# Kernel optimization log

Measured on AMD Instinct MI355X. Metric: run time of the kernel, lower is better.

Reference implementation:

```python
import jax, jax.numpy as jnp
import numpy as np

NL = 64      # layers
NOBS = 400   # observed (velocity, period) pairs
NC = 3000    # trial phase velocities in Clist
DAMP = 1.0


def _var(p, q, ra, rb, wvno, xka, xkb, dpth):
    # surf96 'var': layer eigenfunction products, with c<v / c==v / c>v branches
    ra_s = jnp.where(ra > 0, ra, 1.0)
    rb_s = jnp.where(rb > 0, rb, 1.0)
    # P-wave branch
    sinp = jnp.sin(p)
    facp = jnp.where(p < 16.0, jnp.exp(-2.0 * p), 0.0)
    sinp_e = (1.0 - facp) * 0.5
    ltp = wvno < xka
    eqp = wvno == xka
    pex = jnp.where(ltp | eqp, 0.0, p)
    cosp = jnp.where(ltp, jnp.cos(p), jnp.where(eqp, 1.0, (1.0 + facp) * 0.5))
    w = jnp.where(ltp, sinp / ra_s, jnp.where(eqp, dpth, sinp_e / ra_s))
    x = jnp.where(ltp, -ra * sinp, jnp.where(eqp, 0.0, ra * sinp_e))
    # S-wave branch
    sinq = jnp.sin(q)
    facq = jnp.where(q < 16.0, jnp.exp(-2.0 * q), 0.0)
    sinq_e = (1.0 - facq) * 0.5
    lts = wvno < xkb
    eqs = wvno == xkb
    sex = jnp.where(lts | eqs, 0.0, q)
    cosq = jnp.where(lts, jnp.cos(q), jnp.where(eqs, 1.0, (1.0 + facq) * 0.5))
    y = jnp.where(lts, sinq / rb_s, jnp.where(eqs, dpth, sinq_e / rb_s))
    z = jnp.where(lts, -rb * sinq, jnp.where(eqs, 0.0, rb * sinq_e))

    exa = pex + sex
    a0 = jnp.where(exa < 60.0, jnp.exp(-exa), 0.0)
    return a0, cosp * cosq, cosp * y, cosp * z, cosq * w, cosq * x, x * y, x * z, w * y, w * z


def _dltar4(cvel, tper, d, a, b, rho):
    """Rayleigh dispersion determinant (Dunkin) for a flat batch of (c, T) pairs."""
    omega = jnp.maximum(2.0 * jnp.pi / tper, 1.0e-4)
    wvno = omega / cvel
    wvno2 = wvno * wvno

    def rs(v):
        xk = omega / v
        return xk, jnp.sqrt((wvno + xk) * jnp.abs(wvno - xk))

    # bottom half-space compound E vector
    xka, ra = rs(a[-1])
    xkb, rb = rs(b[-1])
    gammk = 2.0 * (b[-1] / omega) ** 2
    gam = gammk * wvno2
    gamm1 = gam - 1.0
    r = rho[-1]
    e = jnp.stack([
        r * r * (gamm1 * gamm1 - gam * gammk * ra * rb),
        -r * ra,
        r * (gamm1 - gammk * ra * rb),
        r * rb,
        wvno2 - ra * rb,
    ], axis=-1)  # [N,5]

    def step(e, lay):
        dm, am, bm, rm = lay
        xka, ra = rs(am)
        xkb, rb = rs(bm)
        gammk = 2.0 * (bm / omega) ** 2
        gam = gammk * wvno2
        p = ra * dm
        q = rb * dm
        a0, cpcq, cpy, cpz, cqw, cqx, xy, xz, wy, wz = _var(p, q, ra, rb, wvno, xka, xkb, dm)
        gamm1 = gam - 1.0
        twgm1 = gam + gamm1
        gmgmk = gam * gammk
        gmgm1 = gam * gamm1
        gm1sq = gamm1 * gamm1
        rho2 = rm * rm
        a0pq = a0 - cpcq
        t2 = -2.0 * wvno2
        # Dunkin 5x5 compound matrix (surf96 dnka)
        c00 = cpcq - 2.0 * gmgm1 * a0pq - gmgmk * xz - wvno2 * gm1sq * wy
        c01 = (wvno2 * cpy - cqx) / rm
        c02 = -(twgm1 * a0pq + gammk * xz + wvno2 * gamm1 * wy) / rm
        c03 = (cpz - wvno2 * cqw) / rm
        c04 = -(2.0 * wvno2 * a0pq + xz + wvno2 * wvno2 * wy) / rho2
        c10 = (gmgmk * cpz - gm1sq * cqw) * rm
        c11 = cpcq
        c12 = gammk * cpz - gamm1 * cqw
        c13 = -wz
        c14 = c03
        c30 = (gm1sq * cpy - gmgmk * cqx) * rm
        c31 = -xy
        c32 = gamm1 * cpy - gammk * cqx
        c33 = cpcq
        c34 = c01
        c40 = -(2.0 * gmgmk * gm1sq * a0pq + gmgmk * gmgmk * xz + gm1sq * gm1sq * wy) * rho2
        c41 = c30
        c42 = -(gmgm1 * twgm1 * a0pq + gam * gammk * gammk * xz + gamm1 * gm1sq * wy) * rm
        c43 = c10
        c44 = c00
        c20 = t2 * c42
        c21 = t2 * c32
        c22 = a0 + 2.0 * (cpcq - c00)
        c23 = t2 * c12
        c24 = t2 * c02
        ca = jnp.stack([
            jnp.stack([c00, c01, c02, c03, c04], axis=-1),
            jnp.stack([c10, c11, c12, c13, c14], axis=-1),
            jnp.stack([c20, c21, c22, c23, c24], axis=-1),
            jnp.stack([c30, c31, c32, c33, c34], axis=-1),
            jnp.stack([c40, c41, c42, c43, c44], axis=-1),
        ], axis=-2)  # [N,5,5]
        ee = jnp.einsum('nj,nji->ni', e, ca)
        nrm = jnp.max(jnp.abs(ee), axis=-1, keepdims=True)
        nrm = jnp.where(nrm < 1e-30, 1.0, nrm)  # surf96 normc
        return ee / nrm, None

    layers = (d[:-1], a[:-1], b[:-1], rho[:-1])
    e, _ = jax.lax.scan(step, e, layers, reverse=True)  # m = nL-2 ... 0 (llw = -1)
    return e[:, 0]


def _brocher(b):
    a = 0.9409 + 2.0947 * b - 0.8206 * b ** 2 + 0.2683 * b ** 3 - 0.0251 * b ** 4
    rho = 1.6612 * a - 0.4721 * a ** 2 + 0.0671 * a ** 3 - 0.0043 * a ** 4 + 0.000106 * a ** 5
    return a, rho


def _laplacian(n, dtype):
    L = 2.0 * jnp.eye(n, dtype=dtype) - jnp.eye(n, k=1, dtype=dtype) - jnp.eye(n, k=-1, dtype=dtype)
    return L.at[0, 0].set(1.0).at[n - 1, n - 1].set(1.0)


def _forward(vlist, tlist, d, b, Clist):
    a, rho = _brocher(b)  # initial_method='Brocher'
    e00 = _dltar4(vlist, tlist, d, a, b, rho)  # [N]
    # normalization grid: no_grad in original -> stop_gradient on all inputs
    sg = jax.lax.stop_gradient
    nC, nT = Clist.shape[0], tlist.shape[0]
    cgrid = jnp.repeat(Clist, nT)
    tgrid = jnp.tile(tlist, nC)
    det = _dltar4(sg(cgrid), sg(tgrid), sg(d), sg(a), sg(b), sg(rho)).reshape(nC, nT)
    rng = det.max(axis=0) - det.min(axis=0)  # [nT]
    e00 = e00 / rng
    # compress='exp' (torch: 0.1 ** abs(e00) - 1; normalized det branch is unused downstream)
    e00 = jnp.power(jnp.asarray(0.1, e00.dtype), jnp.abs(e00)) - 1.0
    e00_all = jnp.sum(jnp.abs(e00)) / e00.shape[0]
    L = _laplacian(b.shape[0], b.dtype)
    m_norm = DAMP * (L @ b) / b.shape[0]
    return e00_all + jnp.sum(jnp.abs(m_norm))


def setup_inputs() -> dict:
    key = jax.random.key(0)
    k1, k2 = jax.random.split(key)
    tlist = 0.5 + 19.5 * jax.random.uniform(k1, (NOBS,), dtype=jnp.float32)  # periods (s)
    vlist = 1.0 + 3.0 * jax.random.uniform(k2, (NOBS,), dtype=jnp.float32)   # phase velocities (km/s)
    d = jnp.full((NL,), 0.5, dtype=jnp.float32)                              # thicknesses (km)
    b = jnp.linspace(1.0, 4.5, NL, dtype=jnp.float32)                        # Vs profile (km/s)
    Clist = jnp.linspace(1.0, 4.0, NC, dtype=jnp.float32)                    # trial velocities
    return {"vlist": vlist, "tlist": tlist, "d": d, "b": b, "Clist": Clist}


def reference(vlist, tlist, d, b, Clist):
    return _forward(vlist, tlist, d, b, Clist)
```

## Files before the change

### kernel.cpp

```cpp
#include <hip/hip_runtime.h>
#include <math.h>
#include <float.h>

#define NL      64
#define NOBS    400
#define NC      3000
#define HALF_NC 1500
#define CHUNK   64
#define NCHUNK  24
#define TWO_PI_F   6.2831853071795864769f
#define INV_2PI_F  0.15915494309189535f
#define LOG2E_F    1.4426950408889634f
#define LOG2_0P1  -3.3219280948873623f

typedef float fx2 __attribute__((ext_vector_type(2)));

__device__ __forceinline__ float hsin(float x)  { return __builtin_amdgcn_sinf(x); }
__device__ __forceinline__ float hcos(float x)  { return __builtin_amdgcn_cosf(x); }
__device__ __forceinline__ float hexp2(float x) { return __builtin_amdgcn_exp2f(x); }
__device__ __forceinline__ float hrcp(float x)  { return __builtin_amdgcn_rcpf(x); }
__device__ __forceinline__ float hsqrt(float x) { return __builtin_amdgcn_sqrtf(x); }

__device__ __forceinline__ fx2 v_sqrt(fx2 v) { fx2 r; r.x = hsqrt(v.x); r.y = hsqrt(v.y); return r; }
__device__ __forceinline__ fx2 v_rcp (fx2 v) { fx2 r; r.x = hrcp(v.x);  r.y = hrcp(v.y);  return r; }
__device__ __forceinline__ fx2 v_sin (fx2 v) { fx2 r; r.x = hsin(v.x);  r.y = hsin(v.y);  return r; }
__device__ __forceinline__ fx2 v_cos (fx2 v) { fx2 r; r.x = hcos(v.x);  r.y = hcos(v.y);  return r; }
__device__ __forceinline__ fx2 v_exp2(fx2 v) { fx2 r; r.x = hexp2(v.x); r.y = hexp2(v.y); return r; }
__device__ __forceinline__ fx2 v_abs (fx2 v) { fx2 r; r.x = fabsf(v.x); r.y = fabsf(v.y); return r; }
__device__ __forceinline__ fx2 v_max (fx2 a, fx2 b) { fx2 r; r.x = fmaxf(a.x, b.x); r.y = fmaxf(a.y, b.y); return r; }

__device__ __forceinline__ unsigned enc(float f) {
    unsigned u = __float_as_uint(f);
    return (u & 0x80000000u) ? ~u : (u | 0x80000000u);
}
__device__ __forceinline__ float dec(unsigned k) {
    unsigned u = (k & 0x80000000u) ? (k & 0x7fffffffu) : ~k;
    return __uint_as_float(u);
}

__global__ void prep_kernel(const float* __restrict__ b, float* __restrict__ a_out,
                            float* __restrict__ rho_out,
                            unsigned* __restrict__ maxenc, unsigned* __restrict__ minenc) {
    int i = threadIdx.x;
    if (i < NL) {
        float bb = b[i];
        float b2 = bb * bb, b3 = b2 * bb, b4 = b3 * bb;
        float a = 0.9409f + 2.0947f * bb - 0.8206f * b2 + 0.2683f * b3 - 0.0251f * b4;
        float a2 = a * a, a3 = a2 * a, a4 = a3 * a, a5 = a4 * a;
        float rho = 1.6612f * a - 0.4721f * a2 + 0.0671f * a3 - 0.0043f * a4 + 0.000106f * a5;
        a_out[i] = a;
        rho_out[i] = rho;
    }
    for (int j = i; j < NOBS; j += 256) {
        maxenc[j] = 0u;
        minenc[j] = 0xFFFFFFFFu;
    }
}


struct SideVals { float cosv, wv, xv, fv; };

__device__ __forceinline__ SideVals side_mixed(float ra, bool lt, float dmsin,
                                               float dmexp, float ir) {
    float s = hsin(ra * dmsin);
    float c = hcos(ra * dmsin);
    float f = hexp2(ra * dmexp);
    float se = 0.5f - 0.5f * f;
    SideVals r;
    r.cosv = lt ? c : (0.5f + 0.5f * f);
    r.wv = (lt ? s : se) * ir;
    r.xv = ra * (lt ? -s : se);
    r.fv = lt ? 1.0f : f;
    return r;
}

template <bool NORM>
__device__ __forceinline__ void layer_step(
    fx2& f0, fx2& f1, fx2& f2, fx2& f3, fx2& f4,
    const float* __restrict__ P, fx2 wvno2, fx2 t2) {

    float xka2 = P[0], xkb2 = P[1], gammk = P[2];
    float dmsin = P[3], dmexp = P[4];
    float rr = P[5], rr2 = P[6];

    f1 *= rr; f2 *= rr; f3 *= rr; f4 *= rr2;

    fx2 ra2 = wvno2 - xka2;
    fx2 rb2 = wvno2 - xkb2;
    fx2 ra = v_sqrt(v_abs(ra2));
    fx2 rb = v_sqrt(v_abs(rb2));
    fx2 gam = gammk * wvno2;

    bool px = ra2.x < 0.0f, py = ra2.y < 0.0f;
    bool sx = rb2.x < 0.0f, sy = rb2.y < 0.0f;

    fx2 ra_s = v_max(ra, (fx2)1e-18f);
    fx2 rb_s = v_max(rb, (fx2)1e-18f);
    fx2 rp  = v_rcp(ra_s * rb_s);
    fx2 ira = rb_s * rp;
    fx2 irb = ra_s * rp;

    bool allP_prop = __all(px && py);
    bool allP_evan = __all(!(px || py));
    bool allS_prop = __all(sx && sy);
    bool allS_evan = __all(!(sx || sy));

    fx2 cosp, w, x, fp;
    if (allP_prop) {
        fx2 arg = ra * dmsin;
        fx2 s = v_sin(arg);
        cosp = v_cos(arg);
        w = s * ira;
        x = -(ra * s);
        fp = (fx2)1.0f;
    } else if (allP_evan) {
        fx2 f = v_exp2(ra * dmexp);
        fx2 se = 0.5f - 0.5f * f;
        cosp = 0.5f + 0.5f * f;
        w = se * ira;
        x = ra * se;
        fp = f;
    } else {
        SideVals vx = side_mixed(ra.x, px, dmsin, dmexp, ira.x);
        SideVals vy = side_mixed(ra.y, py, dmsin, dmexp, ira.y);
        cosp.x = vx.cosv; w.x = vx.wv; x.x = vx.xv; fp.x = vx.fv;
        cosp.y = vy.cosv; w.y = vy.wv; x.y = vy.xv; fp.y = vy.fv;
    }

    fx2 cosq, y, z, fq;
    if (allS_prop) {
        fx2 arg = rb * dmsin;
        fx2 s = v_sin(arg);
        cosq = v_cos(arg);
        y = s * irb;
        z = -(rb * s);
        fq = (fx2)1.0f;
    } else if (allS_evan) {
        fx2 f = v_exp2(rb * dmexp);
        fx2 se = 0.5f - 0.5f * f;
        cosq = 0.5f + 0.5f * f;
        y = se * irb;
        z = rb * se;
        fq = f;
    } else {
        SideVals vx = side_mixed(rb.x, sx, dmsin, dmexp, irb.x);
        SideVals vy = side_mixed(rb.y, sy, dmsin, dmexp, irb.y);
        cosq.x = vx.cosv; y.x = vx.wv; z.x = vx.xv; fq.x = vx.fv;
        cosq.y = vy.cosv; y.y = vy.wv; z.y = vy.xv; fq.y = vy.fv;
    }

    fx2 a0;
    if (allP_prop && allS_prop) {
        a0 = (fx2)1.0f;
    } else {
        a0 = v_sqrt(fp * fq);
    }

    fx2 cpcq = cosp * cosq;
    fx2 cpy = cosp * y, cpz = cosp * z;
    fx2 cqw = cosq * w, cqx = cosq * x;
    fx2 xy = x * y, xz = x * z, wy = w * y, wz = w * z;

    fx2 gamm1 = gam - 1.0f;
    fx2 twgm1 = gam + gamm1;
    fx2 gmgmk = gam * gammk;
    fx2 gmgm1 = gam * gamm1;
    fx2 gm1sq = gamm1 * gamm1;

    fx2 a0pq  = a0 - cpcq;
    fx2 a0pq2 = a0pq + a0pq;
    fx2 nwy   = wvno2 * wy;
    fx2 gw    = gm1sq * wy;

    fx2 c00  = cpcq - gmgm1 * a0pq2 - gmgmk * xz - gm1sq * nwy;
    fx2 c01  = wvno2 * cpy - cqx;
    fx2 nc02 = twgm1 * a0pq + gammk * xz + gamm1 * nwy;
    fx2 c03  = cpz - wvno2 * cqw;
    fx2 nc04 = wvno2 * a0pq2 + xz + wvno2 * nwy;
    fx2 c10  = gmgmk * cpz - gm1sq * cqw;
    fx2 c12  = gammk * cpz - gamm1 * cqw;
    fx2 c30  = gm1sq * cpy - gmgmk * cqx;
    fx2 c32  = gamm1 * cpy - gammk * cqx;
    fx2 t40  = gm1sq * a0pq2 + gmgmk * xz;
    fx2 nc40 = gmgmk * t40 + gm1sq * gw;
    fx2 th   = gmgm1 * twgm1;
    fx2 nc42 = th * a0pq + (gmgmk * gammk) * xz + gamm1 * gw;
    fx2 c22  = a0 + 2.0f * (cpcq - c00);

    fx2 e2t = f2 * t2;

    fx2 ee0 =  f0 * c00  + f1 * c10  - e2t * nc42 + f3 * c30  - f4 * nc40;
    fx2 ee1 =  f0 * c01  + f1 * cpcq + e2t * c32  - f3 * xy   + f4 * c30;
    fx2 ee2 = -f0 * nc02 + f1 * c12  + f2 * c22   + f3 * c32  - f4 * nc42;
    fx2 ee3 =  f0 * c03  - f1 * wz   + e2t * c12  + f3 * cpcq + f4 * c10;
    fx2 ee4 = -f0 * nc04 + f1 * c03  - e2t * nc02 + f3 * c01  + f4 * c00;

    if (NORM) {
        fx2 nv = v_max(v_max(v_abs(ee0), v_abs(ee1)), v_max(v_abs(ee2), v_abs(ee3)));
        nv = v_max(nv, v_abs(ee4));
        nv = v_max(nv, (fx2)1e-30f);
        fx2 inv;
        inv.x = __uint_as_float(0x7f000000u - (__float_as_uint(nv.x) & 0x7f800000u));
        inv.y = __uint_as_float(0x7f000000u - (__float_as_uint(nv.y) & 0x7f800000u));
        f0 = ee0 * inv; f1 = ee1 * inv; f2 = ee2 * inv; f3 = ee3 * inv; f4 = ee4 * inv;
    } else {
        f0 = ee0; f1 = ee1; f2 = ee2; f3 = ee3; f4 = ee4;
    }
}

__device__ fx2 det_eval(fx2 cvel, float omega, const float* __restrict__ Lf, float ir0) {
    fx2 wvno  = omega * v_rcp(cvel);
    fx2 wvno2 = wvno * wvno;
    fx2 t2    = -2.0f * wvno2;

    const float* P = &Lf[(NL - 1) * 8];
    fx2 ra = v_sqrt(v_abs(wvno2 - P[0]));
    fx2 rb = v_sqrt(v_abs(wvno2 - P[1]));
    float gammk = P[2];
    fx2 gam = gammk * wvno2;
    fx2 gamm1 = gam - 1.0f;
    fx2 rarb = ra * rb;

    fx2 f0 = gamm1 * gamm1 - gam * gammk * rarb;
    fx2 f1 = -ra;
    fx2 f2 = gamm1 - gammk * rarb;
    fx2 f3 = rb;
    fx2 f4 = wvno2 - rarb;

    #pragma unroll 1
    for (int m = NL - 2; m >= 5; m -= 3) {
        layer_step<false>(f0, f1, f2, f3, f4, &Lf[m * 8], wvno2, t2);
        layer_step<false>(f0, f1, f2, f3, f4, &Lf[(m - 1) * 8], wvno2, t2);
        layer_step<true >(f0, f1, f2, f3, f4, &Lf[(m - 2) * 8], wvno2, t2);
    }
    layer_step<false>(f0, f1, f2, f3, f4, &Lf[2 * 8], wvno2, t2);
    layer_step<false>(f0, f1, f2, f3, f4, &Lf[1 * 8], wvno2, t2);
    layer_step<false>(f0, f1, f2, f3, f4, &Lf[0 * 8], wvno2, t2);

    fx2 res;
    {
        float m123 = fmaxf(fmaxf(fabsf(f1.x), fabsf(f2.x)), fabsf(f3.x)) * ir0;
        float nrm = fmaxf(fabsf(f0.x), fmaxf(m123, fabsf(f4.x) * (ir0 * ir0)));
        res.x = f0.x * hrcp(nrm);
    }
    {
        float m123 = fmaxf(fmaxf(fabsf(f1.y), fabsf(f2.y)), fabsf(f3.y)) * ir0;
        float nrm = fmaxf(fabsf(f0.y), fmaxf(m123, fabsf(f4.y) * (ir0 * ir0)));
        res.y = f0.y * hrcp(nrm);
    }
    return res;
}

__global__ __launch_bounds__(64, 2) void det_kernel(
    const float* __restrict__ vlist, const float* __restrict__ tlist,
    const float* __restrict__ d, const float* __restrict__ b,
    const float* __restrict__ Clist,
    const float* __restrict__ a_arr, const float* __restrict__ rho_arr,
    unsigned* __restrict__ maxenc, unsigned* __restrict__ minenc,
    float* __restrict__ e00vals) {

    __shared__ float Lf[NL * 8];
    __shared__ float s_ir0;

    int t     = blockIdx.y;
    int chunk = blockIdx.x;
    int tid   = threadIdx.x;

    float omega = fmaxf(TWO_PI_F / tlist[t], 0.0001f);

    {
        float am = a_arr[tid];
        float bm = b[tid];
        float dm = d[tid];
        float* P = &Lf[tid * 8];
        float ta = omega / am;
        float tb = omega / bm;
        P[0] = ta * ta;
        P[1] = tb * tb;
        float tt = bm / omega;
        P[2] = 2.0f * tt * tt;
        P[3] = dm * INV_2PI_F;
        P[4] = -2.0f * LOG2E_F * dm;
        float rr = (tid < NL - 1) ? (rho_arr[tid] / rho_arr[tid + 1]) : 1.0f;
        P[5] = rr;
        P[6] = rr * rr;
        P[7] = 0.0f;
        if (tid == 0) s_ir0 = 1.0f / rho_arr[0];
    }
    __syncthreads();

    int idx = chunk * CHUNK + tid;
    float lmax = -FLT_MAX, lmin = FLT_MAX;

    if (idx <= HALF_NC) {
        bool grid_pt = idx < HALF_NC;
        fx2 cv;
        if (grid_pt) {
            cv.x = Clist[2 * idx];
            cv.y = Clist[2 * idx + 1];
        } else {
            float v = vlist[t];
            cv.x = v; cv.y = v;
        }
        fx2 det = det_eval(cv, omega, Lf, s_ir0);
        if (grid_pt) {
            lmax = fmaxf(det.x, det.y);
            lmin = fminf(det.x, det.y);
        } else {
            e00vals[t] = det.x;
        }
    }

    #pragma unroll
    for (int off = 32; off >= 1; off >>= 1) {
        lmax = fmaxf(lmax, __shfl_xor(lmax, off));
        lmin = fminf(lmin, __shfl_xor(lmin, off));
    }
    if (tid == 0) {
        atomicMax(&maxenc[t], enc(lmax));
        atomicMin(&minenc[t], enc(lmin));
    }
}

__global__ __launch_bounds__(512) void finalize_kernel(
    const float* __restrict__ b,
    const unsigned* __restrict__ maxenc, const unsigned* __restrict__ minenc,
    const float* __restrict__ e00vals, float* __restrict__ out) {

    int tid = threadIdx.x;
    float acc = 0.0f;

    if (tid < NOBS) {
        float mx = dec(maxenc[tid]);
        float mn = dec(minenc[tid]);
        float rng  = mx - mn;
        float e00  = e00vals[tid] / rng;
        float term = exp2f(LOG2_0P1 * fabsf(e00)) - 1.0f;
        acc = fabsf(term) * (1.0f / (float)NOBS);
    }
    if (tid < NL) {
        float bi = b[tid];
        float lb;
        if (tid == 0)            lb = bi - b[1];
        else if (tid == NL - 1)  lb = bi - b[NL - 2];
        else                     lb = 2.0f * bi - b[tid - 1] - b[tid + 1];
        acc += fabsf(lb * (1.0f / (float)NL));
    }

    __shared__ float s[512];
    s[tid] = acc;
    __syncthreads();
    for (int st = 256; st > 0; st >>= 1) {
        if (tid < st) s[tid] += s[tid + st];
        __syncthreads();
    }
    if (tid == 0) out[0] = s[0];
}

extern "C" void kernel_launch(void* const* d_in, const int* in_sizes, int n_in,
                              void* d_out, int out_size, void* d_ws, size_t ws_size,
                              hipStream_t stream) {
    const float* vlist = (const float*)d_in[0];
    const float* tlist = (const float*)d_in[1];
    const float* d     = (const float*)d_in[2];
    const float* b     = (const float*)d_in[3];
    const float* Clist = (const float*)d_in[4];
    float* out = (float*)d_out;

    float*    ws      = (float*)d_ws;
    float*    a_arr   = ws;
    float*    rho_arr = ws + 64;
    float*    e00v    = ws + 128;
    unsigned* maxenc  = (unsigned*)(ws + 528);
    unsigned* minenc  = (unsigned*)(ws + 928);

    prep_kernel<<<1, 256, 0, stream>>>(b, a_arr, rho_arr, maxenc, minenc);
    det_kernel<<<dim3(NCHUNK, NOBS), 64, 0, stream>>>(vlist, tlist, d, b, Clist,
                                                      a_arr, rho_arr, maxenc, minenc, e00v);
    finalize_kernel<<<1, 512, 0, stream>>>(b, maxenc, minenc, e00v, out);
}
```

Measured before the change: 192.9 us.

## Precompute per-period layer tables in separate kernel, drop LDS staging

Adds a prep2 kernel that builds a per-period layer parameter table (and omega, 1/rho0) in global workspace once per period. Previously each of the 24 chunks recomputed it into shared memory behind a barrier. The det kernel now reads layer parameters directly from global memory, which should hit in cache, instead of from LDS, and no longer needs the __syncthreads. Launch bounds are raised to request more resident waves. The trade-off is an extra kernel launch plus scalar or vector global loads inside the hot layer loop, in place of LDS reads.

```diff
diff --git a/kernel.cpp b/kernel.cpp
--- a/kernel.cpp
+++ b/kernel.cpp
@@ -54,6 +54,33 @@
     for (int j = i; j < NOBS; j += 256) {
         maxenc[j] = 0u;
         minenc[j] = 0xFFFFFFFFu;
+    }
+}
+
+__global__ void prep2_kernel(const float* __restrict__ tlist, const float* __restrict__ d,
+                             const float* __restrict__ b,
+                             const float* __restrict__ a_arr, const float* __restrict__ rho_arr,
+                             float* __restrict__ tabL, float* __restrict__ tab2) {
+    int t = blockIdx.x;
+    int m = threadIdx.x;
+    float omega = fmaxf(TWO_PI_F / tlist[t], 0.0001f);
+    float am = a_arr[m], bm = b[m], dm = d[m];
+    float ta = omega / am;
+    float tb = omega / bm;
+    float tt = bm / omega;
+    float* P = tabL + t * (NL * 8) + m * 8;
+    P[0] = ta * ta;
+    P[1] = tb * tb;
+    P[2] = 2.0f * tt * tt;
+    P[3] = dm * INV_2PI_F;
+    P[4] = -2.0f * LOG2E_F * dm;
+    float rr = (m < NL - 1) ? (rho_arr[m] / rho_arr[m + 1]) : 1.0f;
+    P[5] = rr;
+    P[6] = rr * rr;
+    P[7] = 0.0f;
+    if (m == 0) {
+        tab2[2 * t]     = omega;
+        tab2[2 * t + 1] = 1.0f / rho_arr[0];
     }
 }
 
@@ -208,12 +235,12 @@
     }
 }
 
-__device__ fx2 det_eval(fx2 cvel, float omega, const float* __restrict__ Lf, float ir0) {
+__device__ fx2 det_eval(fx2 cvel, float omega, const float* __restrict__ T, float ir0) {
     fx2 wvno  = omega * v_rcp(cvel);
     fx2 wvno2 = wvno * wvno;
     fx2 t2    = -2.0f * wvno2;
 
-    const float* P = &Lf[(NL - 1) * 8];
+    const float* P = &T[(NL - 1) * 8];
     fx2 ra = v_sqrt(v_abs(wvno2 - P[0]));
     fx2 rb = v_sqrt(v_abs(wvno2 - P[1]));
     float gammk = P[2];
@@ -229,13 +256,13 @@
 
     #pragma unroll 1
     for (int m = NL - 2; m >= 5; m -= 3) {
-        layer_step<false>(f0, f1, f2, f3, f4, &Lf[m * 8], wvno2, t2);
-        layer_step<false>(f0, f1, f2, f3, f4, &Lf[(m - 1) * 8], wvno2, t2);
-        layer_step<true >(f0, f1, f2, f3, f4, &Lf[(m - 2) * 8], wvno2, t2);
-    }
-    layer_step<false>(f0, f1, f2, f3, f4, &Lf[2 * 8], wvno2, t2);
-    layer_step<false>(f0, f1, f2, f3, f4, &Lf[1 * 8], wvno2, t2);
-    layer_step<false>(f0, f1, f2, f3, f4, &Lf[0 * 8], wvno2, t2);
+        layer_step<false>(f0, f1, f2, f3, f4, &T[m * 8], wvno2, t2);
+        layer_step<false>(f0, f1, f2, f3, f4, &T[(m - 1) * 8], wvno2, t2);
+        layer_step<true >(f0, f1, f2, f3, f4, &T[(m - 2) * 8], wvno2, t2);
+    }
+    layer_step<false>(f0, f1, f2, f3, f4, &T[2 * 8], wvno2, t2);
+    layer_step<false>(f0, f1, f2, f3, f4, &T[1 * 8], wvno2, t2);
+    layer_step<false>(f0, f1, f2, f3, f4, &T[0 * 8], wvno2, t2);
 
     fx2 res;
     {
@@ -251,43 +278,19 @@
     return res;
 }
 
-__global__ __launch_bounds__(64, 2) void det_kernel(
-    const float* __restrict__ vlist, const float* __restrict__ tlist,
-    const float* __restrict__ d, const float* __restrict__ b,
-    const float* __restrict__ Clist,
-    const float* __restrict__ a_arr, const float* __restrict__ rho_arr,
+__global__ __launch_bounds__(64, 10) void det_kernel(
+    const float* __restrict__ vlist, const float* __restrict__ Clist,
+    const float* __restrict__ tabL, const float* __restrict__ tab2,
     unsigned* __restrict__ maxenc, unsigned* __restrict__ minenc,
     float* __restrict__ e00vals) {
-
-    __shared__ float Lf[NL * 8];
-    __shared__ float s_ir0;
 
     int t     = blockIdx.y;
     int chunk = blockIdx.x;
     int tid   = threadIdx.x;
 
-    float omega = fmaxf(TWO_PI_F / tlist[t], 0.0001f);
-
-    {
-        float am = a_arr[tid];
-        float bm = b[tid];
-        float dm = d[tid];
-        float* P = &Lf[tid * 8];
-        float ta = omega / am;
-        float tb = omega / bm;
-        P[0] = ta * ta;
-        P[1] = tb * tb;
-        float tt = bm / omega;
-        P[2] = 2.0f * tt * tt;
-        P[3] = dm * INV_2PI_F;
-        P[4] = -2.0f * LOG2E_F * dm;
-        float rr = (tid < NL - 1) ? (rho_arr[tid] / rho_arr[tid + 1]) : 1.0f;
-        P[5] = rr;
-        P[6] = rr * rr;
-        P[7] = 0.0f;
-        if (tid == 0) s_ir0 = 1.0f / rho_arr[0];
-    }
-    __syncthreads();
+    const float* __restrict__ T = tabL + t * (NL * 8);
+    float omega = tab2[2 * t];
+    float ir0   = tab2[2 * t + 1];
 
     int idx = chunk * CHUNK + tid;
     float lmax = -FLT_MAX, lmin = FLT_MAX;
@@ -302,7 +305,7 @@
             float v = vlist[t];
             cv.x = v; cv.y = v;
         }
-        fx2 det = det_eval(cv, omega, Lf, s_ir0);
+        fx2 det = det_eval(cv, omega, T, ir0);
         if (grid_pt) {
             lmax = fmaxf(det.x, det.y);
             lmin = fminf(det.x, det.y);
@@ -373,9 +376,12 @@
     float*    e00v    = ws + 128;
     unsigned* maxenc  = (unsigned*)(ws + 528);
     unsigned* minenc  = (unsigned*)(ws + 928);
+    float*    tab2    = ws + 1328;
+    float*    tabL    = ws + 2128;
 
     prep_kernel<<<1, 256, 0, stream>>>(b, a_arr, rho_arr, maxenc, minenc);
-    det_kernel<<<dim3(NCHUNK, NOBS), 64, 0, stream>>>(vlist, tlist, d, b, Clist,
-                                                      a_arr, rho_arr, maxenc, minenc, e00v);
+    prep2_kernel<<<NOBS, 64, 0, stream>>>(tlist, d, b, a_arr, rho_arr, tabL, tab2);
+    det_kernel<<<dim3(NCHUNK, NOBS), 64, 0, stream>>>(vlist, Clist, tabL, tab2,
+                                                      maxenc, minenc, e00v);
     finalize_kernel<<<1, 512, 0, stream>>>(b, maxenc, minenc, e00v, out);
 }
```

Result: no change. 196.1 us (+1.6%).
